# Kernel optimization log

Measured on AMD Instinct MI355X. Metric: run time of the kernel, lower is better.

## Reference

```python
import jax, jax.numpy as jnp
import numpy as np

N_HEAD = 8
TANH_CLIP = 10.0
NEG = jnp.float32(-1e9)


def setup_inputs() -> dict:
    key = jax.random.key(0)
    ks = jax.random.split(key, 10)
    B, N, E = 128, 1000, 128
    s = lambda k, shape: (jax.random.normal(k, shape, dtype=jnp.float32) * 0.05)
    return dict(
        node_embeddings=s(ks[0], (B, N, E)),
        graph_embedding=s(ks[1], (B, E)),
        Wqkv=s(ks[2], (E, 3 * E)), bqkv=s(ks[3], (3 * E,)),
        Wfix=s(ks[4], (E, E)), bfix=s(ks[5], (E,)),
        Wstep=s(ks[6], (2 * E, E)), bstep=s(ks[7], (E,)),
        Wmlp=s(ks[8], (E, E)), bmlp=s(ks[9], (E,)),
    )


def reference(node_embeddings, graph_embedding, Wqkv, bqkv, Wfix, bfix,
              Wstep, bstep, Wmlp, bmlp):
    B, N, E = node_embeddings.shape
    H = N_HEAD
    d = E // H
    scale = 1.0 / jnp.sqrt(jnp.float32(d))

    # shared projections (done once, like the torch code)
    qkv = node_embeddings @ Wqkv + bqkv               # [B,N,3E]
    k, v, logit_k = jnp.split(qkv, 3, axis=-1)        # each [B,N,E]
    kh = k.reshape(B, N, H, d).transpose(0, 2, 1, 3)  # [B,H,N,d]
    vh = v.reshape(B, N, H, d).transpose(0, 2, 1, 3)  # [B,H,N,d]
    fixed = graph_embedding @ Wfix + bfix             # [B,E]
    first = node_embeddings[:, 0, :]                  # [B,E]

    init_cur = jnp.zeros((B,), jnp.int32)             # depot = node 0
    init_mask = jnp.zeros((B, N), bool).at[:, 0].set(True)  # True = visited/masked
    batch_idx = jnp.arange(B)

    def step(carry, _):
        cur, mask, total = carry
        last = jnp.take_along_axis(node_embeddings, cur[:, None, None], axis=1)[:, 0, :]  # [B,E]
        q = fixed + jnp.concatenate([first, last], axis=-1) @ Wstep + bstep               # [B,E]
        qh = q.reshape(B, H, d)
        attn = jnp.einsum('bhd,bhnd->bhn', qh, kh) * scale
        attn = jnp.where(mask[:, None, :], NEG, attn)
        attn = jax.nn.softmax(attn, axis=-1)
        ctx = jnp.einsum('bhn,bhnd->bhd', attn, vh).reshape(B, E)
        x = ctx @ Wmlp + bmlp
        logits = jnp.einsum('be,bne->bn', x, logit_k) * scale
        logits = jnp.tanh(logits) * TANH_CLIP
        logits = jnp.where(mask, NEG, logits)
        log_p = jax.nn.log_softmax(logits, axis=-1)
        act = jnp.argmax(log_p, axis=-1).astype(jnp.int32)   # greedy decode
        lp = jnp.take_along_axis(log_p, act[:, None], axis=-1)[:, 0]
        new_mask = mask.at[batch_idx, act].set(True)
        return (act, new_mask, total + lp), act

    (cur, mask, total), seq = jax.lax.scan(
        step, (init_cur, init_mask, jnp.zeros((B,), jnp.float32)), None, length=N - 1)
    # total: summed log-prob of selected tour, [B] (matches _log_p_ in torch code)
    return total
```

## Files before the change

### kernel.cpp

```cpp
#include <hip/hip_runtime.h>
#include <hip/hip_fp16.h>

constexpr int kB = 128;
constexpr int kN = 1000;
constexpr int kE = 128;
constexpr int kH = 8;
constexpr float kFP8Scale = 64.f;
constexpr float kQKScale = 0.25f / 64.f;

typedef _Float16 h2 __attribute__((ext_vector_type(2)));
typedef float f2 __attribute__((ext_vector_type(2)));

__device__ __forceinline__ h2 pkrtz(float a, float b) {
  return __builtin_bit_cast(h2, __builtin_amdgcn_cvt_pkrtz(a, b));
}

__device__ __forceinline__ float dotq(unsigned u, h2 qa, h2 qb, float s) {
  f2 lo = __builtin_amdgcn_cvt_pk_f32_fp8(u, false);
  f2 hi = __builtin_amdgcn_cvt_pk_f32_fp8(u, true);
  h2 l16 = pkrtz(lo.x, lo.y);
  h2 h16 = pkrtz(hi.x, hi.y);
  s = __builtin_amdgcn_fdot2(l16, qa, s, false);
  s = __builtin_amdgcn_fdot2(h16, qb, s, false);
  return s;
}
__device__ __forceinline__ float dot16(uint4 tq, const h2* q8, float s) {
  s = dotq(tq.x, q8[0], q8[1], s);
  s = dotq(tq.y, q8[2], q8[3], s);
  s = dotq(tq.z, q8[4], q8[5], s);
  s = dotq(tq.w, q8[6], q8[7], s);
  return s;
}

__device__ __forceinline__ float fast_tanh(float x) {
  float t = __expf(2.f * x);
  return 1.f - 2.f / (t + 1.f);
}

__device__ __forceinline__ unsigned char enc_fp8(float v) {
  unsigned p = __builtin_amdgcn_cvt_pk_fp8_f32(v, v, 0, false);
  return (unsigned char)(p & 0xFF);
}

__device__ __forceinline__ void combine(float& m, float& s, int& a,
                                        float mo, float so, int ao) {
  bool take = (mo > m) || (mo == m && ao < a);
  float mw = take ? mo : m;
  float ml = take ? m : mo;
  float sw = take ? so : s;
  float sl = take ? s : so;
  s = sw + sl * __expf(ml - mw);
  m = mw;
  a = take ? ao : a;
}

template <int CTRL>
__device__ __forceinline__ float dpp_bcastf(float x) {
  return __builtin_bit_cast(
      float, __builtin_amdgcn_update_dpp(0, __builtin_bit_cast(int, x), CTRL,
                                         0xf, 0xf, true));
}
template <int CTRL>
__device__ __forceinline__ int dpp_bcasti(int x) {
  return __builtin_amdgcn_update_dpp(0, x, CTRL, 0xf, 0xf, true);
}
template <int CTRL>
__device__ __forceinline__ float dpp_addf(float x) {
  return x + dpp_bcastf<CTRL>(x);
}
template <int CTRL>
__device__ __forceinline__ void dpp_combine(float& m, float& s, int& a) {
  float mo = dpp_bcastf<CTRL>(m);
  float so = dpp_bcastf<CTRL>(s);
  int ao = dpp_bcasti<CTRL>(a);
  combine(m, s, a, mo, so, ao);
}

__device__ __forceinline__ void barrier_lds() {
  asm volatile("s_waitcnt lgkmcnt(0)" ::: "memory");
  __builtin_amdgcn_s_barrier();
  asm volatile("" ::: "memory");
}

__global__ __launch_bounds__(384) void qkv_kernel(
    const float* __restrict__ ne, const float* __restrict__ Wqkv,
    const float* __restrict__ bqkv, unsigned char* __restrict__ kq,
    unsigned char* __restrict__ vq, unsigned char* __restrict__ lkq) {
  __shared__ float rows[16 * kE];
  int b = blockIdx.x;
  int n0 = blockIdx.y * 16;
  int ntile = min(16, kN - n0);
  int tid = threadIdx.x;

  for (int idx = tid; idx < ntile * kE; idx += 384)
    rows[idx] = ne[(b * kN + n0) * kE + idx];
  __syncthreads();

  int j = tid;
  float acc[16];
#pragma unroll
  for (int r = 0; r < 16; ++r) acc[r] = 0.f;
  for (int i = 0; i < kE; ++i) {
    float w = Wqkv[i * (3 * kE) + j];
#pragma unroll
    for (int r = 0; r < 16; ++r) acc[r] += rows[r * kE + i] * w;
  }
  float bias = bqkv[j];
  unsigned char* dst;
  int col;
  if (j < kE) { dst = kq; col = j; }
  else if (j < 2 * kE) { dst = vq; col = j - kE; }
  else { dst = lkq; col = j - 2 * kE; }
  for (int r = 0; r < ntile; ++r)
    dst[(size_t)(b * kN + n0 + r) * kE + col] =
        enc_fp8((acc[r] + bias) * kFP8Scale);
}

__global__ __launch_bounds__(128) void qbase_kernel(
    const float* __restrict__ ne, const float* __restrict__ ge,
    const float* __restrict__ Wfix, const float* __restrict__ bfix,
    const float* __restrict__ Wstep, const float* __restrict__ bstep,
    float* __restrict__ qbase) {
  __shared__ float g[kE], f[kE];
  int b = blockIdx.x, e = threadIdx.x;
  g[e] = ge[b * kE + e];
  f[e] = ne[(size_t)b * kN * kE + e];
  __syncthreads();
  float acc = bfix[e] + bstep[e];
  for (int i = 0; i < kE; ++i)
    acc += g[i] * Wfix[i * kE + e] + f[i] * Wstep[i * kE + e];
  qbase[b * kE + e] = acc;
}

__global__ __launch_bounds__(128) void qstep_kernel(
    const float* __restrict__ ne, const float* __restrict__ Wstep,
    const float* __restrict__ qbase, __half* __restrict__ qstep) {
  __shared__ float rows[8 * kE];
  int b = blockIdx.x;
  int n0 = blockIdx.y * 8;
  int tid = threadIdx.x;
  const float* Wbot = Wstep + kE * kE;

  for (int idx = tid; idx < 8 * kE; idx += 128)
    rows[idx] = ne[((size_t)b * kN + n0) * kE + idx];
  __syncthreads();

  float acc[8];
#pragma unroll
  for (int r = 0; r < 8; ++r) acc[r] = 0.f;
  for (int i = 0; i < kE; ++i) {
    float w = Wbot[i * kE + tid];
#pragma unroll
    for (int r = 0; r < 8; ++r) acc[r] += rows[r * kE + i] * w;
  }
  float qb = qbase[b * kE + tid];
#pragma unroll
  for (int r = 0; r < 8; ++r)
    qstep[((size_t)b * kN + n0 + r) * kE + tid] =
        __float2half((qb + acc[r]) * kQKScale);
}

__global__ __launch_bounds__(1024) void rollout_kernel(
    const float* __restrict__ Wmlp, const float* __restrict__ bmlp,
    const unsigned char* __restrict__ kq, const unsigned char* __restrict__ vq,
    const unsigned char* __restrict__ lkq, const __half* __restrict__ qstep,
    float* __restrict__ out) {
  __shared__ __align__(16) int rem[1024];
  __shared__ __align__(16) float parts[kE][65];
  __shared__ __align__(16) float wmT[kE][132];
  __shared__ float bm[kE];
  __shared__ __align__(16) float ctx[kE];
  __shared__ __align__(16) __half xh[kE];
  __shared__ float redSum[16][kH];
  __shared__ __align__(16) float4 redPack[16];

  int b = blockIdx.x;
  int tid = threadIdx.x;
  int lane = tid & 63;
  int wave = tid >> 6;
  int g = tid >> 3;
  int t = tid & 7;

  const unsigned char* kqb = kq + (size_t)b * kN * kE;
  const unsigned char* vqb = vq + (size_t)b * kN * kE;
  const unsigned char* lqb = lkq + (size_t)b * kN * kE;
  const __half* qsb = qstep + (size_t)b * kN * kE;

#pragma unroll
  for (int m = 0; m < 16; ++m) {
    int idx = tid * 16 + m;
    wmT[idx & 127][idx >> 7] = Wmlp[idx];
  }
  rem[tid] = (tid < kN - 1) ? tid + 1 : kN - 1;
  if (tid < kE) bm[tid] = bmlp[tid];

  int A = 0;
  uint4 qa, qb_;
  {
    const uint4* qr = (const uint4*)qsb;
    qa = qr[2 * t];
    qb_ = qr[2 * t + 1];
  }
  float total = 0.f;

  barrier_lds();

  for (int step = 0; step < kN - 1; ++step) {
    int R = kN - 1 - step;

    int jn[8];
#pragma unroll
    for (int r = 0; r < 8; ++r) {
      int j = g + 128 * r;
      jn[r] = (j < R) ? rem[j] : -1;
    }
    h2 q8[8];
    {
      unsigned qw[8] = {qa.x, qa.y, qa.z, qa.w, qb_.x, qb_.y, qb_.z, qb_.w};
#pragma unroll
      for (int i = 0; i < 8; ++i) q8[i] = __builtin_bit_cast(h2, qw[i]);
    }
    uint4 kb0, vb0, kb1, vb1;
    if (jn[0] >= 0) {
      kb0 = ((const uint4*)(kqb + (size_t)jn[0] * kE))[t];
      vb0 = ((const uint4*)(vqb + (size_t)jn[0] * kE))[t];
    }
    if (jn[1] >= 0) {
      kb1 = ((const uint4*)(kqb + (size_t)jn[1] * kE))[t];
      vb1 = ((const uint4*)(vqb + (size_t)jn[1] * kE))[t];
    }
    float acc[16];
#pragma unroll
    for (int i = 0; i < 16; ++i) acc[i] = 0.f;
    float den = 0.f;
#pragma unroll
    for (int r = 0; r < 8; ++r) {
      if (jn[r] < 0) break;
      uint4 kk = (r & 1) ? kb1 : kb0;
      uint4 vv = (r & 1) ? vb1 : vb0;
      if (r + 2 < 8 && jn[r + 2] >= 0) {
        if (r & 1) {
          kb1 = ((const uint4*)(kqb + (size_t)jn[r + 2] * kE))[t];
          vb1 = ((const uint4*)(vqb + (size_t)jn[r + 2] * kE))[t];
        } else {
          kb0 = ((const uint4*)(kqb + (size_t)jn[r + 2] * kE))[t];
          vb0 = ((const uint4*)(vqb + (size_t)jn[r + 2] * kE))[t];
        }
      }
      float s = dot16(kk, q8, 0.f);
      float hv = __expf(s);
      den += hv;
      unsigned uu[4] = {vv.x, vv.y, vv.z, vv.w};
#pragma unroll
      for (int c = 0; c < 4; ++c) {
        f2 lo = __builtin_amdgcn_cvt_pk_f32_fp8(uu[c], false);
        f2 hi = __builtin_amdgcn_cvt_pk_f32_fp8(uu[c], true);
        acc[4 * c + 0] += hv * lo.x;
        acc[4 * c + 1] += hv * lo.y;
        acc[4 * c + 2] += hv * hi.x;
        acc[4 * c + 3] += hv * hi.y;
      }
    }
    den = dpp_addf<0x128>(den);
    den += __shfl_xor(den, 16);
    den += __shfl_xor(den, 32);
    if (lane < kH) redSum[wave][lane] = den;
#pragma unroll
    for (int i = 0; i < 16; ++i) acc[i] = dpp_addf<0x128>(acc[i]);
    if (((lane >> 3) & 1) == 0) {
      int chunk = wave * 4 + (lane >> 4);
#pragma unroll
      for (int i = 0; i < 16; ++i)
        parts[t * 16 + i][(chunk + 4 * t) & 63] = acc[i];
    }
    uint4 lu[8];
#pragma unroll
    for (int r = 0; r < 8; ++r)
      if (jn[r] >= 0) lu[r] = ((const uint4*)(lqb + (size_t)jn[r] * kE))[t];
    barrier_lds();

    {
      int e = tid >> 3, k = tid & 7, hh = e >> 4;
      float s = 0.f;
#pragma unroll
      for (int m = 0; m < 8; ++m)
        s += parts[e][((8 * k + m) + 4 * hh) & 63];
      float d = redSum[2 * k][hh] + redSum[2 * k + 1][hh];
      s = dpp_addf<0xB1>(s);
      s = dpp_addf<0x4E>(s);
      s = dpp_addf<0x141>(s);
      d = dpp_addf<0xB1>(d);
      d = dpp_addf<0x4E>(d);
      d = dpp_addf<0x141>(d);
      if (k == 0) ctx[e] = s / (d * kFP8Scale);
    }
    barrier_lds();

    {
      float xacc = 0.f;
      const float4* c4 = (const float4*)(ctx + t * 16);
      const float4* w4 = (const float4*)(&wmT[g][t * 16]);
#pragma unroll
      for (int k4 = 0; k4 < 4; ++k4) {
        float4 cv = c4[k4];
        float4 wv = w4[k4];
        xacc += cv.x * wv.x + cv.y * wv.y + cv.z * wv.z + cv.w * wv.w;
      }
      xacc = dpp_addf<0xB1>(xacc);
      xacc = dpp_addf<0x4E>(xacc);
      xacc = dpp_addf<0x141>(xacc);
      if (t == 0) xh[g] = __float2half((bm[g] + xacc) * kQKScale);
    }
    barrier_lds();

    int myv = rem[tid];
    int nxt = rem[(tid < 1023) ? tid + 1 : 1023];
    float m = -1e30f, ssum = 0.f;
    int arg = 0x7fffffff;
    {
      h2 x8[8];
      uint4 xv0 = ((const uint4*)xh)[2 * t];
      uint4 xv1 = ((const uint4*)xh)[2 * t + 1];
      unsigned xw[8] = {xv0.x, xv0.y, xv0.z, xv0.w,
                        xv1.x, xv1.y, xv1.z, xv1.w};
#pragma unroll
      for (int i = 0; i < 8; ++i) x8[i] = __builtin_bit_cast(h2, xw[i]);
#pragma unroll
      for (int r = 0; r < 8; ++r)
        if (jn[r] >= 0) {
          float s = dot16(lu[r], x8, 0.f);
          s = dpp_addf<0xB1>(s);
          s = dpp_addf<0x4E>(s);
          s = dpp_addf<0x141>(s);
          if (t == r) {
            m = fast_tanh(s) * 10.f;
            ssum = 1.f;
            arg = jn[r];
          }
        }
    }
    dpp_combine<0xB1>(m, ssum, arg);
    dpp_combine<0x4E>(m, ssum, arg);
    dpp_combine<0x141>(m, ssum, arg);
    dpp_combine<0x128>(m, ssum, arg);
#pragma unroll
    for (int off = 16; off <= 32; off <<= 1) {
      float mo = __shfl_xor(m, off);
      float so = __shfl_xor(ssum, off);
      int ao = __shfl_xor(arg, off);
      combine(m, ssum, arg, mo, so, ao);
    }
    if (lane == 0)
      redPack[wave] = make_float4(m, ssum, __int_as_float(arg), 0.f);
    barrier_lds();

    {
      float4 rp = redPack[lane & 15];
      float M = rp.x, S = rp.y;
      int Af = __float_as_int(rp.z);
      dpp_combine<0xB1>(M, S, Af);
      dpp_combine<0x4E>(M, S, Af);
      dpp_combine<0x141>(M, S, Af);
      dpp_combine<0x128>(M, S, Af);
      A = Af;
      total += -logf(S);
      const uint4* qr = (const uint4*)(qsb + (size_t)A * kE);
      qa = qr[2 * t];
      qb_ = qr[2 * t + 1];
      if (tid < R - 1 && myv >= A) rem[tid] = nxt;
    }
    barrier_lds();
  }
  if (tid == 0) out[b] = total;
}

extern "C" void kernel_launch(void* const* d_in, const int* in_sizes, int n_in,
                              void* d_out, int out_size, void* d_ws,
                              size_t ws_size, hipStream_t stream) {
  const float* ne = (const float*)d_in[0];
  const float* ge = (const float*)d_in[1];
  const float* Wqkv = (const float*)d_in[2];
  const float* bqkv = (const float*)d_in[3];
  const float* Wfix = (const float*)d_in[4];
  const float* bfix = (const float*)d_in[5];
  const float* Wstep = (const float*)d_in[6];
  const float* bstep = (const float*)d_in[7];
  const float* Wmlp = (const float*)d_in[8];
  const float* bmlp = (const float*)d_in[9];
  float* out = (float*)d_out;

  size_t nkv = (size_t)kB * kN * kE;
  unsigned char* kq = (unsigned char*)d_ws;
  unsigned char* vq = kq + nkv;
  unsigned char* lkq = vq + nkv;
  __half* qstep = (__half*)(lkq + nkv);
  float* qbase = (float*)(qstep + nkv);

  qkv_kernel<<<dim3(kB, (kN + 15) / 16), 384, 0, stream>>>(ne, Wqkv, bqkv, kq,
                                                           vq, lkq);
  qbase_kernel<<<kB, kE, 0, stream>>>(ne, ge, Wfix, bfix, Wstep, bstep, qbase);
  qstep_kernel<<<dim3(kB, kN / 8), 128, 0, stream>>>(ne, Wstep, qbase, qstep);
  rollout_kernel<<<kB, 1024, 0, stream>>>(Wmlp, bmlp, kq, vq, lkq, qstep, out);
}
```

Baseline: 8.664 ms.

## Prefetch next step's first K/V rows across the step barrier and hoist logit-key loads

```diff
diff --git a/kernel.cpp b/kernel.cpp
--- a/kernel.cpp
+++ b/kernel.cpp
@@ -167,7 +167,7 @@
     float* __restrict__ out) {
   __shared__ __align__(16) int rem[1024];
   __shared__ __align__(16) float parts[kE][65];
-  __shared__ __align__(16) float wmT[kE][132];
+  __shared__ __align__(16) float wmT[kE][140];
   __shared__ float bm[kE];
   __shared__ __align__(16) float ctx[kE];
   __shared__ __align__(16) __half xh[kE];
@@ -205,12 +205,26 @@
 
   barrier_lds();
 
+  int pjn0 = (g < kN - 1) ? g + 1 : -1;
+  int pjn1 = (g + 128 < kN - 1) ? g + 129 : -1;
+  uint4 kb0, vb0, kb1, vb1;
+  if (pjn0 >= 0) {
+    kb0 = ((const uint4*)(kqb + (size_t)pjn0 * kE))[t];
+    vb0 = ((const uint4*)(vqb + (size_t)pjn0 * kE))[t];
+  }
+  if (pjn1 >= 0) {
+    kb1 = ((const uint4*)(kqb + (size_t)pjn1 * kE))[t];
+    vb1 = ((const uint4*)(vqb + (size_t)pjn1 * kE))[t];
+  }
+
   for (int step = 0; step < kN - 1; ++step) {
     int R = kN - 1 - step;
 
     int jn[8];
-#pragma unroll
-    for (int r = 0; r < 8; ++r) {
+    jn[0] = pjn0;
+    jn[1] = pjn1;
+#pragma unroll
+    for (int r = 2; r < 8; ++r) {
       int j = g + 128 * r;
       jn[r] = (j < R) ? rem[j] : -1;
     }
@@ -219,15 +233,6 @@
       unsigned qw[8] = {qa.x, qa.y, qa.z, qa.w, qb_.x, qb_.y, qb_.z, qb_.w};
 #pragma unroll
       for (int i = 0; i < 8; ++i) q8[i] = __builtin_bit_cast(h2, qw[i]);
-    }
-    uint4 kb0, vb0, kb1, vb1;
-    if (jn[0] >= 0) {
-      kb0 = ((const uint4*)(kqb + (size_t)jn[0] * kE))[t];
-      vb0 = ((const uint4*)(vqb + (size_t)jn[0] * kE))[t];
-    }
-    if (jn[1] >= 0) {
-      kb1 = ((const uint4*)(kqb + (size_t)jn[1] * kE))[t];
-      vb1 = ((const uint4*)(vqb + (size_t)jn[1] * kE))[t];
     }
     float acc[16];
 #pragma unroll
@@ -261,6 +266,10 @@
         acc[4 * c + 3] += hv * hi.y;
       }
     }
+    uint4 lu[8];
+#pragma unroll
+    for (int r = 0; r < 8; ++r)
+      if (jn[r] >= 0) lu[r] = ((const uint4*)(lqb + (size_t)jn[r] * kE))[t];
     den = dpp_addf<0x128>(den);
     den += __shfl_xor(den, 16);
     den += __shfl_xor(den, 32);
@@ -273,10 +282,6 @@
       for (int i = 0; i < 16; ++i)
         parts[t * 16 + i][(chunk + 4 * t) & 63] = acc[i];
     }
-    uint4 lu[8];
-#pragma unroll
-    for (int r = 0; r < 8; ++r)
-      if (jn[r] >= 0) lu[r] = ((const uint4*)(lqb + (size_t)jn[r] * kE))[t];
     barrier_lds();
 
     {
@@ -315,6 +320,10 @@
 
     int myv = rem[tid];
     int nxt = rem[(tid < 1023) ? tid + 1 : 1023];
+    int pr0 = rem[g];
+    int pr1 = rem[g + 1];
+    int pr2 = rem[g + 128];
+    int pr3 = rem[g + 129];
     float m = -1e30f, ssum = 0.f;
     int arg = 0x7fffffff;
     {
@@ -367,6 +376,17 @@
       const uint4* qr = (const uint4*)(qsb + (size_t)A * kE);
       qa = qr[2 * t];
       qb_ = qr[2 * t + 1];
+      int Rn = R - 1;
+      pjn0 = (g < Rn) ? ((pr0 < A) ? pr0 : pr1) : -1;
+      pjn1 = (g + 128 < Rn) ? ((pr2 < A) ? pr2 : pr3) : -1;
+      if (pjn0 >= 0) {
+        kb0 = ((const uint4*)(kqb + (size_t)pjn0 * kE))[t];
+        vb0 = ((const uint4*)(vqb + (size_t)pjn0 * kE))[t];
+      }
+      if (pjn1 >= 0) {
+        kb1 = ((const uint4*)(kqb + (size_t)pjn1 * kE))[t];
+        vb1 = ((const uint4*)(vqb + (size_t)pjn1 * kE))[t];
+      }
       if (tid < R - 1 && myv >= A) rem[tid] = nxt;
     }
     barrier_lds();
```

New measurement: 8.657 ms. About the same (-0.1%).

## Precompute next remaining-node indices in registers and drop per-step trailing barrier

Applied to the files above, without the earlier changes.

```diff
diff --git a/kernel.cpp b/kernel.cpp
--- a/kernel.cpp
+++ b/kernel.cpp
@@ -11,27 +11,6 @@
 typedef _Float16 h2 __attribute__((ext_vector_type(2)));
 typedef float f2 __attribute__((ext_vector_type(2)));
 
-__device__ __forceinline__ h2 pkrtz(float a, float b) {
-  return __builtin_bit_cast(h2, __builtin_amdgcn_cvt_pkrtz(a, b));
-}
-
-__device__ __forceinline__ float dotq(unsigned u, h2 qa, h2 qb, float s) {
-  f2 lo = __builtin_amdgcn_cvt_pk_f32_fp8(u, false);
-  f2 hi = __builtin_amdgcn_cvt_pk_f32_fp8(u, true);
-  h2 l16 = pkrtz(lo.x, lo.y);
-  h2 h16 = pkrtz(hi.x, hi.y);
-  s = __builtin_amdgcn_fdot2(l16, qa, s, false);
-  s = __builtin_amdgcn_fdot2(h16, qb, s, false);
-  return s;
-}
-__device__ __forceinline__ float dot16(uint4 tq, const h2* q8, float s) {
-  s = dotq(tq.x, q8[0], q8[1], s);
-  s = dotq(tq.y, q8[2], q8[3], s);
-  s = dotq(tq.z, q8[4], q8[5], s);
-  s = dotq(tq.w, q8[6], q8[7], s);
-  return s;
-}
-
 __device__ __forceinline__ float fast_tanh(float x) {
   float t = __expf(2.f * x);
   return 1.f - 2.f / (t + 1.f);
@@ -42,15 +21,38 @@
   return (unsigned char)(p & 0xFF);
 }
 
-__device__ __forceinline__ void combine(float& m, float& s, int& a,
-                                        float mo, float so, int ao) {
+__device__ __forceinline__ void dotp(unsigned u, f2 qa, f2 qb, f2& sacc) {
+  f2 lo = __builtin_amdgcn_cvt_pk_f32_fp8(u, false);
+  f2 hi = __builtin_amdgcn_cvt_pk_f32_fp8(u, true);
+  sacc += lo * qa;
+  sacc += hi * qb;
+}
+__device__ __forceinline__ float dot16p(uint4 tq, const f2* q2) {
+  f2 s = {0.f, 0.f};
+  dotp(tq.x, q2[0], q2[1], s);
+  dotp(tq.y, q2[2], q2[3], s);
+  dotp(tq.z, q2[4], q2[5], s);
+  dotp(tq.w, q2[6], q2[7], s);
+  return s.x + s.y;
+}
+__device__ __forceinline__ void vaccp(unsigned u, f2 hv2, f2& a0, f2& a1) {
+  f2 lo = __builtin_amdgcn_cvt_pk_f32_fp8(u, false);
+  f2 hi = __builtin_amdgcn_cvt_pk_f32_fp8(u, true);
+  a0 += hv2 * lo;
+  a1 += hv2 * hi;
+}
+__device__ __forceinline__ void unpack16(uint4 a, uint4 b, f2* q2) {
+  unsigned w[8] = {a.x, a.y, a.z, a.w, b.x, b.y, b.z, b.w};
+#pragma unroll
+  for (int i = 0; i < 8; ++i) {
+    h2 hh = __builtin_bit_cast(h2, w[i]);
+    q2[i] = f2{(float)hh.x, (float)hh.y};
+  }
+}
+
+__device__ __forceinline__ void maxcomb(float& m, int& a, float mo, int ao) {
   bool take = (mo > m) || (mo == m && ao < a);
-  float mw = take ? mo : m;
-  float ml = take ? m : mo;
-  float sw = take ? so : s;
-  float sl = take ? s : so;
-  s = sw + sl * __expf(ml - mw);
-  m = mw;
+  m = take ? mo : m;
   a = take ? ao : a;
 }
 
@@ -69,11 +71,10 @@
   return x + dpp_bcastf<CTRL>(x);
 }
 template <int CTRL>
-__device__ __forceinline__ void dpp_combine(float& m, float& s, int& a) {
+__device__ __forceinline__ void dpp_maxcomb(float& m, int& a) {
   float mo = dpp_bcastf<CTRL>(m);
-  float so = dpp_bcastf<CTRL>(s);
   int ao = dpp_bcasti<CTRL>(a);
-  combine(m, s, a, mo, so, ao);
+  maxcomb(m, a, mo, ao);
 }
 
 __device__ __forceinline__ void barrier_lds() {
@@ -167,7 +168,7 @@
     float* __restrict__ out) {
   __shared__ __align__(16) int rem[1024];
   __shared__ __align__(16) float parts[kE][65];
-  __shared__ __align__(16) float wmT[kE][132];
+  __shared__ __align__(16) float wmT[kE][140];
   __shared__ float bm[kE];
   __shared__ __align__(16) float ctx[kE];
   __shared__ __align__(16) __half xh[kE];
@@ -203,23 +204,18 @@
   }
   float total = 0.f;
 
+  int jn[8];
+#pragma unroll
+  for (int r = 0; r < 8; ++r) {
+    int j = g + 128 * r;
+    jn[r] = (j < kN - 1) ? j + 1 : -1;
+  }
+
   barrier_lds();
 
   for (int step = 0; step < kN - 1; ++step) {
     int R = kN - 1 - step;
 
-    int jn[8];
-#pragma unroll
-    for (int r = 0; r < 8; ++r) {
-      int j = g + 128 * r;
-      jn[r] = (j < R) ? rem[j] : -1;
-    }
-    h2 q8[8];
-    {
-      unsigned qw[8] = {qa.x, qa.y, qa.z, qa.w, qb_.x, qb_.y, qb_.z, qb_.w};
-#pragma unroll
-      for (int i = 0; i < 8; ++i) q8[i] = __builtin_bit_cast(h2, qw[i]);
-    }
     uint4 kb0, vb0, kb1, vb1;
     if (jn[0] >= 0) {
       kb0 = ((const uint4*)(kqb + (size_t)jn[0] * kE))[t];
@@ -229,9 +225,11 @@
       kb1 = ((const uint4*)(kqb + (size_t)jn[1] * kE))[t];
       vb1 = ((const uint4*)(vqb + (size_t)jn[1] * kE))[t];
     }
-    float acc[16];
-#pragma unroll
-    for (int i = 0; i < 16; ++i) acc[i] = 0.f;
+    f2 q2[8];
+    unpack16(qa, qb_, q2);
+    f2 acc2[8];
+#pragma unroll
+    for (int i = 0; i < 8; ++i) acc2[i] = f2{0.f, 0.f};
     float den = 0.f;
 #pragma unroll
     for (int r = 0; r < 8; ++r) {
@@ -247,36 +245,41 @@
           vb0 = ((const uint4*)(vqb + (size_t)jn[r + 2] * kE))[t];
         }
       }
-      float s = dot16(kk, q8, 0.f);
+      float s = dot16p(kk, q2);
       float hv = __expf(s);
       den += hv;
-      unsigned uu[4] = {vv.x, vv.y, vv.z, vv.w};
-#pragma unroll
-      for (int c = 0; c < 4; ++c) {
-        f2 lo = __builtin_amdgcn_cvt_pk_f32_fp8(uu[c], false);
-        f2 hi = __builtin_amdgcn_cvt_pk_f32_fp8(uu[c], true);
-        acc[4 * c + 0] += hv * lo.x;
-        acc[4 * c + 1] += hv * lo.y;
-        acc[4 * c + 2] += hv * hi.x;
-        acc[4 * c + 3] += hv * hi.y;
-      }
-    }
+      f2 hv2 = {hv, hv};
+      vaccp(vv.x, hv2, acc2[0], acc2[1]);
+      vaccp(vv.y, hv2, acc2[2], acc2[3]);
+      vaccp(vv.z, hv2, acc2[4], acc2[5]);
+      vaccp(vv.w, hv2, acc2[6], acc2[7]);
+    }
+    uint4 lu[8];
+#pragma unroll
+    for (int r = 0; r < 8; ++r)
+      if (jn[r] >= 0) lu[r] = ((const uint4*)(lqb + (size_t)jn[r] * kE))[t];
     den = dpp_addf<0x128>(den);
     den += __shfl_xor(den, 16);
     den += __shfl_xor(den, 32);
     if (lane < kH) redSum[wave][lane] = den;
-#pragma unroll
-    for (int i = 0; i < 16; ++i) acc[i] = dpp_addf<0x128>(acc[i]);
-    if (((lane >> 3) & 1) == 0) {
-      int chunk = wave * 4 + (lane >> 4);
-#pragma unroll
-      for (int i = 0; i < 16; ++i)
-        parts[t * 16 + i][(chunk + 4 * t) & 63] = acc[i];
-    }
-    uint4 lu[8];
-#pragma unroll
-    for (int r = 0; r < 8; ++r)
-      if (jn[r] >= 0) lu[r] = ((const uint4*)(lqb + (size_t)jn[r] * kE))[t];
+    {
+      float av[16];
+#pragma unroll
+      for (int c = 0; c < 4; ++c) {
+        av[4 * c + 0] = acc2[2 * c].x;
+        av[4 * c + 1] = acc2[2 * c].y;
+        av[4 * c + 2] = acc2[2 * c + 1].x;
+        av[4 * c + 3] = acc2[2 * c + 1].y;
+      }
+#pragma unroll
+      for (int i = 0; i < 16; ++i) av[i] = dpp_addf<0x128>(av[i]);
+      if (((lane >> 3) & 1) == 0) {
+        int chunk = wave * 4 + (lane >> 4);
+#pragma unroll
+        for (int i = 0; i < 16; ++i)
+          parts[t * 16 + i][(chunk + 4 * t) & 63] = av[i];
+      }
+    }
     barrier_lds();
 
     {
@@ -315,61 +318,84 @@
 
     int myv = rem[tid];
     int nxt = rem[(tid < 1023) ? tid + 1 : 1023];
-    float m = -1e30f, ssum = 0.f;
+    int pra[8], prb[8];
+#pragma unroll
+    for (int r = 0; r < 8; ++r) {
+      int j = g + 128 * r;
+      pra[r] = rem[j];
+      prb[r] = rem[(j < 1023) ? j + 1 : 1023];
+    }
+    float m0 = -1e30f;
     int arg = 0x7fffffff;
     {
-      h2 x8[8];
+      f2 x2[8];
       uint4 xv0 = ((const uint4*)xh)[2 * t];
       uint4 xv1 = ((const uint4*)xh)[2 * t + 1];
-      unsigned xw[8] = {xv0.x, xv0.y, xv0.z, xv0.w,
-                        xv1.x, xv1.y, xv1.z, xv1.w};
-#pragma unroll
-      for (int i = 0; i < 8; ++i) x8[i] = __builtin_bit_cast(h2, xw[i]);
+      unpack16(xv0, xv1, x2);
 #pragma unroll
       for (int r = 0; r < 8; ++r)
         if (jn[r] >= 0) {
-          float s = dot16(lu[r], x8, 0.f);
+          float s = dot16p(lu[r], x2);
           s = dpp_addf<0xB1>(s);
           s = dpp_addf<0x4E>(s);
           s = dpp_addf<0x141>(s);
           if (t == r) {
-            m = fast_tanh(s) * 10.f;
-            ssum = 1.f;
+            m0 = fast_tanh(s) * 10.f;
             arg = jn[r];
           }
         }
     }
-    dpp_combine<0xB1>(m, ssum, arg);
-    dpp_combine<0x4E>(m, ssum, arg);
-    dpp_combine<0x141>(m, ssum, arg);
-    dpp_combine<0x128>(m, ssum, arg);
+    float M = m0;
+    int argM = arg;
+    dpp_maxcomb<0xB1>(M, argM);
+    dpp_maxcomb<0x4E>(M, argM);
+    dpp_maxcomb<0x141>(M, argM);
+    dpp_maxcomb<0x128>(M, argM);
 #pragma unroll
     for (int off = 16; off <= 32; off <<= 1) {
-      float mo = __shfl_xor(m, off);
-      float so = __shfl_xor(ssum, off);
-      int ao = __shfl_xor(arg, off);
-      combine(m, ssum, arg, mo, so, ao);
-    }
+      float mo = __shfl_xor(M, off);
+      int ao = __shfl_xor(argM, off);
+      maxcomb(M, argM, mo, ao);
+    }
+    float ex = __expf(m0 - M);
+    ex = dpp_addf<0xB1>(ex);
+    ex = dpp_addf<0x4E>(ex);
+    ex = dpp_addf<0x141>(ex);
+    ex = dpp_addf<0x128>(ex);
+    ex += __shfl_xor(ex, 16);
+    ex += __shfl_xor(ex, 32);
     if (lane == 0)
-      redPack[wave] = make_float4(m, ssum, __int_as_float(arg), 0.f);
+      redPack[wave] = make_float4(M, ex, __int_as_float(argM), 0.f);
     barrier_lds();
 
     {
       float4 rp = redPack[lane & 15];
-      float M = rp.x, S = rp.y;
-      int Af = __float_as_int(rp.z);
-      dpp_combine<0xB1>(M, S, Af);
-      dpp_combine<0x4E>(M, S, Af);
-      dpp_combine<0x141>(M, S, Af);
-      dpp_combine<0x128>(M, S, Af);
+      float mw = rp.x, sw = rp.y;
+      int aw = __float_as_int(rp.z);
+      float Mf = mw;
+      int Af = aw;
+      dpp_maxcomb<0xB1>(Mf, Af);
+      dpp_maxcomb<0x4E>(Mf, Af);
+      dpp_maxcomb<0x141>(Mf, Af);
+      dpp_maxcomb<0x128>(Mf, Af);
+      float sc = sw * __expf(mw - Mf);
+      sc = dpp_addf<0xB1>(sc);
+      sc = dpp_addf<0x4E>(sc);
+      sc = dpp_addf<0x141>(sc);
+      sc = dpp_addf<0x128>(sc);
       A = Af;
-      total += -logf(S);
+      total += -logf(sc);
       const uint4* qr = (const uint4*)(qsb + (size_t)A * kE);
       qa = qr[2 * t];
       qb_ = qr[2 * t + 1];
+      int Rn = R - 1;
+#pragma unroll
+      for (int r = 0; r < 8; ++r) {
+        int j = g + 128 * r;
+        jn[r] = (j < Rn) ? ((pra[r] < A) ? pra[r] : prb[r]) : -1;
+      }
       if (tid < R - 1 && myv >= A) rem[tid] = nxt;
     }
-    barrier_lds();
   }
   if (tid == 0) out[b] = total;
 }
```

Result: no change. 8.684 ms (+0.2%).
